# Performance work log

Measured on AMD Instinct MI355X. Metric: run time of the kernel, lower is better.

## Reference

```python
import jax, jax.numpy as jnp
import numpy as np

B, L, D = 4, 2048, 256
H, HD = 8, 64
MAX_LEN = 2048


def setup_inputs() -> dict:
    key = jax.random.key(0)
    ks = jax.random.split(key, 5)
    x = jax.random.normal(ks[0], (B, L, D), dtype=jnp.float32)
    glorot_q = (2.0 / (D + H * HD)) ** 0.5
    Wq = jax.random.normal(ks[1], (D, H * HD), dtype=jnp.float32) * glorot_q
    Wk = jax.random.normal(ks[2], (D, H * HD), dtype=jnp.float32) * glorot_q
    bq = jnp.zeros((H, 1, 1, HD), dtype=jnp.float32)
    bk = jnp.zeros((H, 1, 1, HD), dtype=jnp.float32)
    prior_mean = jax.random.uniform(ks[3], (H,), dtype=jnp.float32, minval=-1.0, maxval=1.0)
    log_prior_std = jnp.full((H,), np.log(0.4), dtype=jnp.float32)
    return {"x": x, "Wq": Wq, "bq": bq, "Wk": Wk, "bk": bk,
            "prior_mean": prior_mean, "log_prior_std": log_prior_std,
            "max_length": MAX_LEN}


def _gaussian(x, mean, std):
    return 1.0 / std / jnp.sqrt(2.0 * 3.1415926) * jnp.exp(-0.5 * (x - mean) ** 2 / std ** 2)


def reference(x, Wq, bq, Wk, bk, prior_mean, log_prior_std, max_length):
    b, l, d = x.shape
    h, hd = bq.shape[0], bq.shape[-1]
    # normalized signed distance matrix [l, l]
    r = jnp.arange(l, dtype=jnp.float32)
    dist = (r[None, :] - r[:, None]) / float(max_length)
    # projections -> [h, b, l, hd] (split heads along last dim, heads leading)
    q = (x @ Wq).reshape(b, l, h, hd).transpose(2, 0, 1, 3) + bq
    k = (x @ Wk).reshape(b, l, h, hd).transpose(2, 0, 1, 3) + bk
    # gaussian positional prior per head [h, l, l]
    prior = _gaussian(dist[None, :, :], prior_mean[:, None, None],
                      jnp.exp(log_prior_std)[:, None, None])
    # scaled QK^T * prior -> softmax over keys
    scores = jnp.einsum('hbqd,hbkd->hbqk', q, k) * (float(hd) ** -0.5)
    att = jax.nn.softmax(scores * prior[:, None, :, :], axis=-1)
    # distance-weighted reduction instead of V-matmul: [h, b, l] -> [b, l, h]
    distance = jnp.einsum('hbqk,qk->hbq', att, dist)
    return distance.transpose(1, 2, 0)
```

## Files before the change

kernel.cpp:

```cpp
#include <hip/hip_runtime.h>
#include <math.h>


#define B_  4
#define L_  2048
#define D_  256
#define H_  8
#define HD_ 64

typedef unsigned int u32;
typedef unsigned short u16;
typedef short bf16x8 __attribute__((ext_vector_type(8)));
typedef float f32x4  __attribute__((ext_vector_type(4)));

union U16x8 { u16 u[8]; bf16x8 v; uint4 q; };

__device__ __forceinline__ u16 bf16rne(float v) {
    u32 u = __float_as_uint(v);
    return (u16)((u + 0x7fffu + ((u >> 16) & 1u)) >> 16);
}
__device__ __forceinline__ float bf2f(u16 h) { return __uint_as_float(((u32)h) << 16); }

__global__ __launch_bounds__(256, 4) void proj_kernel(
    const float* __restrict__ x,
    const float* __restrict__ Wq, const float* __restrict__ bq,
    const float* __restrict__ Wk, const float* __restrict__ bk,
    u16* __restrict__ Qhi, u16* __restrict__ Qlo,
    u16* __restrict__ Khi, u16* __restrict__ Klo)
{
    __shared__ __align__(16) u16 Bs[2][64][40];

    const int z = blockIdx.z;
    const float* W    = z ? Wk : Wq;
    const float* bias = z ? bk : bq;
    u16* Ohi = z ? Khi : Qhi;
    u16* Olo = z ? Klo : Qlo;

    const int t = threadIdx.x, w = t >> 6, l = t & 63;
    const int kc = l & 15, lhi = l >> 4;
    const int m0 = blockIdx.x * 128 + w * 32;
    const int h  = blockIdx.y;

    const float* xp0 = x + (size_t)(m0 + kc) * D_;
    const float* xp1 = x + (size_t)(m0 + 16 + kc) * D_;

    f32x4 acc[2][4];
    #pragma unroll
    for (int mf = 0; mf < 2; ++mf)
        #pragma unroll
        for (int nf = 0; nf < 4; ++nf) acc[mf][nf] = (f32x4){0.f, 0.f, 0.f, 0.f};

    for (int ks = 0; ks < 8; ++ks) {
        __syncthreads();
        #pragma unroll
        for (int j = 0; j < 2; ++j) {
            const int fid = t + j * 256;
            const int kr = fid >> 4, c4 = fid & 15;
            float4 v = *(const float4*)&W[(size_t)(ks*32 + kr) * 512 + h*64 + c4*4];
            float vv[4] = {v.x, v.y, v.z, v.w};
            #pragma unroll
            for (int e = 0; e < 4; ++e) {
                const int n = c4*4 + e;
                const u16 hi = bf16rne(vv[e]);
                Bs[0][n][kr] = hi;
                Bs[1][n][kr] = bf16rne(vv[e] - bf2f(hi));
            }
        }
        __syncthreads();

        U16x8 ah[2], al[2];
        #pragma unroll
        for (int mf = 0; mf < 2; ++mf) {
            const float* xp = mf ? xp1 : xp0;
            float4 a = *(const float4*)(xp + ks*32 + lhi*8);
            float4 b = *(const float4*)(xp + ks*32 + lhi*8 + 4);
            float vv[8] = {a.x, a.y, a.z, a.w, b.x, b.y, b.z, b.w};
            #pragma unroll
            for (int e = 0; e < 8; ++e) {
                const u16 hi = bf16rne(vv[e]);
                ah[mf].u[e] = hi;
                al[mf].u[e] = bf16rne(vv[e] - bf2f(hi));
            }
        }

        #pragma unroll
        for (int nf = 0; nf < 4; ++nf) {
            const bf16x8 bh = *(const bf16x8*)&Bs[0][nf*16 + kc][lhi*8];
            const bf16x8 bl = *(const bf16x8*)&Bs[1][nf*16 + kc][lhi*8];
            #pragma unroll
            for (int mf = 0; mf < 2; ++mf) {
                acc[mf][nf] = __builtin_amdgcn_mfma_f32_16x16x32_bf16(ah[mf].v, bh, acc[mf][nf], 0, 0, 0);
                acc[mf][nf] = __builtin_amdgcn_mfma_f32_16x16x32_bf16(ah[mf].v, bl, acc[mf][nf], 0, 0, 0);
                acc[mf][nf] = __builtin_amdgcn_mfma_f32_16x16x32_bf16(al[mf].v, bh, acc[mf][nf], 0, 0, 0);
            }
        }
    }

    #pragma unroll
    for (int mf = 0; mf < 2; ++mf)
        #pragma unroll
        for (int nf = 0; nf < 4; ++nf) {
            const float bv = bias[h * 64 + nf*16 + kc];
            #pragma unroll
            for (int r = 0; r < 4; ++r) {
                const float v = acc[mf][nf][r] + bv;
                const u16 hi = bf16rne(v);
                const u16 lo = bf16rne(v - bf2f(hi));
                const int m = m0 + mf*16 + lhi*4 + r;
                const int bb = m >> 11, ll = m & (L_ - 1);
                const size_t o = (((size_t)h * B_ + bb) * L_ + ll) * HD_ + nf*16 + kc;
                Ohi[o] = hi; Olo[o] = lo;
            }
        }
}

__global__ __launch_bounds__(512, 4) void attn_kernel(
    const u16* __restrict__ Qhi, const u16* __restrict__ Qlo,
    const u16* __restrict__ Khi, const u16* __restrict__ Klo,
    const float* __restrict__ prior_mean, const float* __restrict__ log_prior_std,
    const int* __restrict__ max_len, float* __restrict__ out)
{
    __shared__ __align__(16) u16 kls[2][64 * 64];
    __shared__ float2 Ptab[2176];

    const int t = threadIdx.x, w = t >> 6, l = t & 63;
    const int kc = l & 15, lhi = l >> 4;
    const int q0 = blockIdx.x * 128;
    const int hb = blockIdx.y, h = hb >> 2, b = hb & 3;
    const int qw = q0 + w * 16;

    const float iml = 1.0f / (float)(*max_len);
    const float mu  = prior_mean[h];
    const float sg  = __expf(log_prior_std[h]);
    const float isg = 1.0f / sg;
    const float coef = 0.125f / (sg * 2.5066282746310002f) * 1.44269504089f;
    for (int i = t; i < 2175; i += 512) {
        const float dist = (float)(i - q0 - 127) * iml;
        const float tt = (dist - mu) * isg;
        Ptab[i] = make_float2(coef * __expf(-0.5f * tt * tt), dist);
    }

    bf16x8 qh[2], ql2[2];
    #pragma unroll
    for (int dh = 0; dh < 2; ++dh) {
        const size_t qo = ((size_t)hb * L_ + qw + kc) * HD_ + dh*32 + lhi*8;
        qh[dh]  = *(const bf16x8*)&Qhi[qo];
        ql2[dh] = *(const bf16x8*)&Qlo[qo];
    }

    const float2* pbase = &Ptab[lhi*4 + 127 - w*16 - kc];

    const int spl = t >> 8;
    const int srow = (t & 255) >> 2;
    const int sq = t & 3;
    const int sr7 = srow & 7;
    const u16* Kg = (spl ? Klo : Khi) + ((size_t)hb * L_ + srow) * HD_ + sq * 16;
    u16* lds_row = &kls[spl][srow * 64];

    const int sl0 = lhi ^ (l & 7);
    const int sl1 = (4 + lhi) ^ (l & 7);

    float lv = 0.f, wv = 0.f;

    for (int kt = 0; kt < 32; ++kt) {
        __syncthreads();
        {
            const u16* src = Kg + (size_t)kt * 64 * HD_;
            const uint4 g0 = *(const uint4*)src;
            const uint4 g1 = *(const uint4*)(src + 8);
            const int p0 = (sq*2)     ^ sr7;
            const int p1 = (sq*2 + 1) ^ sr7;
            *(uint4*)&lds_row[p0 * 8] = g0;
            *(uint4*)&lds_row[p1 * 8] = g1;
        }
        __syncthreads();

        f32x4 acc[4];
        #pragma unroll
        for (int kf = 0; kf < 4; ++kf) acc[kf] = (f32x4){0.f, 0.f, 0.f, 0.f};

        #pragma unroll
        for (int kf = 0; kf < 4; ++kf) {
            const int rbase = (kf*16 + kc) * 64;
            const bf16x8 ah0 = *(const bf16x8*)&kls[0][rbase + sl0*8];
            const bf16x8 ah1 = *(const bf16x8*)&kls[0][rbase + sl1*8];
            const bf16x8 al0 = *(const bf16x8*)&kls[1][rbase + sl0*8];
            const bf16x8 al1 = *(const bf16x8*)&kls[1][rbase + sl1*8];
            acc[kf] = __builtin_amdgcn_mfma_f32_16x16x32_bf16(ah0, qh[0],  acc[kf], 0, 0, 0);
            acc[kf] = __builtin_amdgcn_mfma_f32_16x16x32_bf16(ah1, qh[1],  acc[kf], 0, 0, 0);
            acc[kf] = __builtin_amdgcn_mfma_f32_16x16x32_bf16(ah0, ql2[0], acc[kf], 0, 0, 0);
            acc[kf] = __builtin_amdgcn_mfma_f32_16x16x32_bf16(ah1, ql2[1], acc[kf], 0, 0, 0);
            acc[kf] = __builtin_amdgcn_mfma_f32_16x16x32_bf16(al0, qh[0],  acc[kf], 0, 0, 0);
            acc[kf] = __builtin_amdgcn_mfma_f32_16x16x32_bf16(al1, qh[1],  acc[kf], 0, 0, 0);
        }

        const float2* pp = pbase + kt * 64;
        #pragma unroll
        for (int kf = 0; kf < 4; ++kf)
            #pragma unroll
            for (int r = 0; r < 4; ++r) {
                const float2 pd = pp[kf*16 + r];
                const float e = exp2f(acc[kf][r] * pd.x);
                lv += e;
                wv = fmaf(e, pd.y, wv);
            }
    }

    lv += __shfl_xor(lv, 16); wv += __shfl_xor(wv, 16);
    lv += __shfl_xor(lv, 32); wv += __shfl_xor(wv, 32);
    if (lhi == 0) {
        const int q = qw + kc;
        out[((size_t)(b * L_ + q)) * H_ + h] = wv / lv;
    }
}

extern "C" void kernel_launch(void* const* d_in, const int* in_sizes, int n_in,
                              void* d_out, int out_size, void* d_ws, size_t ws_size,
                              hipStream_t stream)
{
    const float* x   = (const float*)d_in[0];
    const float* Wq  = (const float*)d_in[1];
    const float* bq  = (const float*)d_in[2];
    const float* Wk  = (const float*)d_in[3];
    const float* bk  = (const float*)d_in[4];
    const float* pm  = (const float*)d_in[5];
    const float* lps = (const float*)d_in[6];
    const int*   mlp = (const int*)d_in[7];
    float* out = (float*)d_out;

    u16* Qhi = (u16*)d_ws;
    u16* Qlo = Qhi + 4194304;
    u16* Khi = Qlo + 4194304;
    u16* Klo = Khi + 4194304;

    proj_kernel<<<dim3(64, 8, 2), 256, 0, stream>>>(x, Wq, bq, Wk, bk, Qhi, Qlo, Khi, Klo);
    attn_kernel<<<dim3(16, 32), 512, 0, stream>>>(Qhi, Qlo, Khi, Klo, pm, lps, mlp, out);
}
```

Before: 163.4 us.

## Pre-split x/W to bf16 pairs, double-buffer K tiles, remap blocks per XCD

A new prep kernel converts x and a transposed W into bf16 hi/lo pairs once, so the projection kernel reads them straight from global memory with no LDS staging or per-block conversion. This path is taken only when the workspace is large enough, otherwise the old projection kernel runs. The attention kernel double-buffers K tiles in LDS with register prefetch and one barrier per tile. It also drops the distance table by computing the weighted sum algebraically, uses a raw exp2 builtin with setprio around the MFMA block, and remaps block indices so each XCD handles contiguous head/batch work. Together these cut LDS traffic and conversion work, at the cost of an extra launch, more workspace and more LDS.

```diff
diff --git a/kernel.cpp b/kernel.cpp
--- a/kernel.cpp
+++ b/kernel.cpp
@@ -13,36 +13,92 @@
 typedef short bf16x8 __attribute__((ext_vector_type(8)));
 typedef float f32x4  __attribute__((ext_vector_type(4)));
 
-union U16x8 { u16 u[8]; bf16x8 v; uint4 q; };
-
 __device__ __forceinline__ u16 bf16rne(float v) {
     u32 u = __float_as_uint(v);
     return (u16)((u + 0x7fffu + ((u >> 16) & 1u)) >> 16);
 }
 __device__ __forceinline__ float bf2f(u16 h) { return __uint_as_float(((u32)h) << 16); }
 
-__global__ __launch_bounds__(256, 4) void proj_kernel(
-    const float* __restrict__ x,
-    const float* __restrict__ Wq, const float* __restrict__ bq,
-    const float* __restrict__ Wk, const float* __restrict__ bk,
+#if __has_builtin(__builtin_amdgcn_exp2f)
+__device__ __forceinline__ float fast_exp2(float x) { return __builtin_amdgcn_exp2f(x); }
+#else
+__device__ __forceinline__ float fast_exp2(float x) { return exp2f(x); }
+#endif
+
+__global__ __launch_bounds__(256) void prep_kernel(
+    const float* __restrict__ x, const float* __restrict__ Wq, const float* __restrict__ Wk,
+    u16* __restrict__ xhi, u16* __restrict__ xlo,
+    u16* __restrict__ wthi, u16* __restrict__ wtlo)
+{
+    __shared__ float Ws[64][65];
+    const int t = threadIdx.x;
+    if (blockIdx.x < 1024) {
+        const size_t base = ((size_t)blockIdx.x * 256 + t) * 8;
+        float4 a = *(const float4*)&x[base];
+        float4 b = *(const float4*)&x[base + 4];
+        float v[8] = {a.x, a.y, a.z, a.w, b.x, b.y, b.z, b.w};
+        u32 hp[4], lp[4];
+        #pragma unroll
+        for (int j = 0; j < 4; ++j) {
+            u16 h0 = bf16rne(v[2*j]),   l0 = bf16rne(v[2*j]   - bf2f(bf16rne(v[2*j])));
+            u16 h1 = bf16rne(v[2*j+1]), l1 = bf16rne(v[2*j+1] - bf2f(bf16rne(v[2*j+1])));
+            hp[j] = (u32)h0 | ((u32)h1 << 16);
+            lp[j] = (u32)l0 | ((u32)l1 << 16);
+        }
+        *(uint4*)&xhi[base] = *(uint4*)hp;
+        *(uint4*)&xlo[base] = *(uint4*)lp;
+    } else {
+        const int widx = blockIdx.x - 1024;
+        const int wsel = widx >> 5;
+        const float* W = wsel ? Wk : Wq;
+        const int tile = widx & 31;
+        const int kt = tile >> 3, nt = tile & 7;
+        const int kr = t >> 2, c4 = t & 3;
+        #pragma unroll
+        for (int c = 0; c < 4; ++c) {
+            float4 v = *(const float4*)&W[(size_t)(kt*64 + kr) * 512 + nt*64 + c4*16 + c*4];
+            Ws[kr][c4*16 + c*4 + 0] = v.x; Ws[kr][c4*16 + c*4 + 1] = v.y;
+            Ws[kr][c4*16 + c*4 + 2] = v.z; Ws[kr][c4*16 + c*4 + 3] = v.w;
+        }
+        __syncthreads();
+        const int nr = t >> 2;
+        const int kc4 = (t & 3) * 16;
+        u32 hp[8], lp[8];
+        #pragma unroll
+        for (int j = 0; j < 8; ++j) {
+            float v0 = Ws[kc4 + 2*j][nr], v1 = Ws[kc4 + 2*j + 1][nr];
+            u16 h0 = bf16rne(v0), h1 = bf16rne(v1);
+            u16 l0 = bf16rne(v0 - bf2f(h0)), l1 = bf16rne(v1 - bf2f(h1));
+            hp[j] = (u32)h0 | ((u32)h1 << 16);
+            lp[j] = (u32)l0 | ((u32)l1 << 16);
+        }
+        const size_t ob = ((size_t)wsel*512 + nt*64 + nr) * 256 + kt*64 + kc4;
+        *(uint4*)&wthi[ob] = *(uint4*)&hp[0]; *(uint4*)&wthi[ob + 8] = *(uint4*)&hp[4];
+        *(uint4*)&wtlo[ob] = *(uint4*)&lp[0]; *(uint4*)&wtlo[ob + 8] = *(uint4*)&lp[4];
+    }
+}
+
+__global__ __launch_bounds__(256, 4) void projA_kernel(
+    const u16* __restrict__ xhi, const u16* __restrict__ xlo,
+    const u16* __restrict__ wthi, const u16* __restrict__ wtlo,
+    const float* __restrict__ bq, const float* __restrict__ bk,
     u16* __restrict__ Qhi, u16* __restrict__ Qlo,
     u16* __restrict__ Khi, u16* __restrict__ Klo)
 {
-    __shared__ __align__(16) u16 Bs[2][64][40];
-
-    const int z = blockIdx.z;
-    const float* W    = z ? Wk : Wq;
+    const int p = blockIdx.x;
+    const int xcd = p & 7, s = p >> 3;
+    const int mx = xcd * 8 + (s & 7);
+    const int hz = s >> 3;
+    const int h = hz & 7, z = hz >> 3;
+
     const float* bias = z ? bk : bq;
     u16* Ohi = z ? Khi : Qhi;
     u16* Olo = z ? Klo : Qlo;
 
     const int t = threadIdx.x, w = t >> 6, l = t & 63;
     const int kc = l & 15, lhi = l >> 4;
-    const int m0 = blockIdx.x * 128 + w * 32;
-    const int h  = blockIdx.y;
-
-    const float* xp0 = x + (size_t)(m0 + kc) * D_;
-    const float* xp1 = x + (size_t)(m0 + 16 + kc) * D_;
+    const int m0 = mx * 128 + w * 32;
+    const size_t wb = ((size_t)z * 512 + h * 64) * 256;
 
     f32x4 acc[2][4];
     #pragma unroll
@@ -50,50 +106,30 @@
         #pragma unroll
         for (int nf = 0; nf < 4; ++nf) acc[mf][nf] = (f32x4){0.f, 0.f, 0.f, 0.f};
 
+    #pragma unroll 2
     for (int ks = 0; ks < 8; ++ks) {
-        __syncthreads();
-        #pragma unroll
-        for (int j = 0; j < 2; ++j) {
-            const int fid = t + j * 256;
-            const int kr = fid >> 4, c4 = fid & 15;
-            float4 v = *(const float4*)&W[(size_t)(ks*32 + kr) * 512 + h*64 + c4*4];
-            float vv[4] = {v.x, v.y, v.z, v.w};
-            #pragma unroll
-            for (int e = 0; e < 4; ++e) {
-                const int n = c4*4 + e;
-                const u16 hi = bf16rne(vv[e]);
-                Bs[0][n][kr] = hi;
-                Bs[1][n][kr] = bf16rne(vv[e] - bf2f(hi));
-            }
-        }
-        __syncthreads();
-
-        U16x8 ah[2], al[2];
+        const int ko = ks * 32 + lhi * 8;
+        bf16x8 ah[2], al[2], bh[4], bl[4];
         #pragma unroll
         for (int mf = 0; mf < 2; ++mf) {
-            const float* xp = mf ? xp1 : xp0;
-            float4 a = *(const float4*)(xp + ks*32 + lhi*8);
-            float4 b = *(const float4*)(xp + ks*32 + lhi*8 + 4);
-            float vv[8] = {a.x, a.y, a.z, a.w, b.x, b.y, b.z, b.w};
-            #pragma unroll
-            for (int e = 0; e < 8; ++e) {
-                const u16 hi = bf16rne(vv[e]);
-                ah[mf].u[e] = hi;
-                al[mf].u[e] = bf16rne(vv[e] - bf2f(hi));
-            }
-        }
-
+            const size_t ao = (size_t)(m0 + mf*16 + kc) * 256 + ko;
+            ah[mf] = *(const bf16x8*)&xhi[ao];
+            al[mf] = *(const bf16x8*)&xlo[ao];
+        }
         #pragma unroll
         for (int nf = 0; nf < 4; ++nf) {
-            const bf16x8 bh = *(const bf16x8*)&Bs[0][nf*16 + kc][lhi*8];
-            const bf16x8 bl = *(const bf16x8*)&Bs[1][nf*16 + kc][lhi*8];
-            #pragma unroll
-            for (int mf = 0; mf < 2; ++mf) {
-                acc[mf][nf] = __builtin_amdgcn_mfma_f32_16x16x32_bf16(ah[mf].v, bh, acc[mf][nf], 0, 0, 0);
-                acc[mf][nf] = __builtin_amdgcn_mfma_f32_16x16x32_bf16(ah[mf].v, bl, acc[mf][nf], 0, 0, 0);
-                acc[mf][nf] = __builtin_amdgcn_mfma_f32_16x16x32_bf16(al[mf].v, bh, acc[mf][nf], 0, 0, 0);
-            }
-        }
+            const size_t bo = wb + (size_t)(nf*16 + kc) * 256 + ko;
+            bh[nf] = *(const bf16x8*)&wthi[bo];
+            bl[nf] = *(const bf16x8*)&wtlo[bo];
+        }
+        #pragma unroll
+        for (int mf = 0; mf < 2; ++mf)
+            #pragma unroll
+            for (int nf = 0; nf < 4; ++nf) {
+                acc[mf][nf] = __builtin_amdgcn_mfma_f32_16x16x32_bf16(ah[mf], bh[nf], acc[mf][nf], 0, 0, 0);
+                acc[mf][nf] = __builtin_amdgcn_mfma_f32_16x16x32_bf16(ah[mf], bl[nf], acc[mf][nf], 0, 0, 0);
+                acc[mf][nf] = __builtin_amdgcn_mfma_f32_16x16x32_bf16(al[mf], bh[nf], acc[mf][nf], 0, 0, 0);
+            }
     }
 
     #pragma unroll
@@ -114,30 +150,127 @@
         }
 }
 
+__global__ __launch_bounds__(256, 4) void projB_kernel(
+    const float* __restrict__ x,
+    const float* __restrict__ Wq, const float* __restrict__ bq,
+    const float* __restrict__ Wk, const float* __restrict__ bk,
+    u16* __restrict__ Qhi, u16* __restrict__ Qlo,
+    u16* __restrict__ Khi, u16* __restrict__ Klo)
+{
+    __shared__ __align__(16) u16 Bs[2][64][40];
+
+    const int z = blockIdx.z;
+    const float* W    = z ? Wk : Wq;
+    const float* bias = z ? bk : bq;
+    u16* Ohi = z ? Khi : Qhi;
+    u16* Olo = z ? Klo : Qlo;
+
+    const int t = threadIdx.x, w = t >> 6, l = t & 63;
+    const int kc = l & 15, lhi = l >> 4;
+    const int m0 = blockIdx.x * 128 + w * 32;
+    const int h  = blockIdx.y;
+
+    const float* xp0 = x + (size_t)(m0 + kc) * D_;
+    const float* xp1 = x + (size_t)(m0 + 16 + kc) * D_;
+
+    f32x4 acc[2][4];
+    #pragma unroll
+    for (int mf = 0; mf < 2; ++mf)
+        #pragma unroll
+        for (int nf = 0; nf < 4; ++nf) acc[mf][nf] = (f32x4){0.f, 0.f, 0.f, 0.f};
+
+    for (int ks = 0; ks < 8; ++ks) {
+        __syncthreads();
+        #pragma unroll
+        for (int j = 0; j < 2; ++j) {
+            const int fid = t + j * 256;
+            const int kr = fid >> 4, c4 = fid & 15;
+            float4 v = *(const float4*)&W[(size_t)(ks*32 + kr) * 512 + h*64 + c4*4];
+            float vv[4] = {v.x, v.y, v.z, v.w};
+            #pragma unroll
+            for (int e = 0; e < 4; ++e) {
+                const int n = c4*4 + e;
+                const u16 hi = bf16rne(vv[e]);
+                Bs[0][n][kr] = hi;
+                Bs[1][n][kr] = bf16rne(vv[e] - bf2f(hi));
+            }
+        }
+        __syncthreads();
+
+        union { u16 u[8]; bf16x8 v; } ah[2], al[2];
+        #pragma unroll
+        for (int mf = 0; mf < 2; ++mf) {
+            const float* xp = mf ? xp1 : xp0;
+            float4 a = *(const float4*)(xp + ks*32 + lhi*8);
+            float4 b = *(const float4*)(xp + ks*32 + lhi*8 + 4);
+            float vv[8] = {a.x, a.y, a.z, a.w, b.x, b.y, b.z, b.w};
+            #pragma unroll
+            for (int e = 0; e < 8; ++e) {
+                const u16 hi = bf16rne(vv[e]);
+                ah[mf].u[e] = hi;
+                al[mf].u[e] = bf16rne(vv[e] - bf2f(hi));
+            }
+        }
+
+        #pragma unroll
+        for (int nf = 0; nf < 4; ++nf) {
+            const bf16x8 bh = *(const bf16x8*)&Bs[0][nf*16 + kc][lhi*8];
+            const bf16x8 bl = *(const bf16x8*)&Bs[1][nf*16 + kc][lhi*8];
+            #pragma unroll
+            for (int mf = 0; mf < 2; ++mf) {
+                acc[mf][nf] = __builtin_amdgcn_mfma_f32_16x16x32_bf16(ah[mf].v, bh, acc[mf][nf], 0, 0, 0);
+                acc[mf][nf] = __builtin_amdgcn_mfma_f32_16x16x32_bf16(ah[mf].v, bl, acc[mf][nf], 0, 0, 0);
+                acc[mf][nf] = __builtin_amdgcn_mfma_f32_16x16x32_bf16(al[mf].v, bh, acc[mf][nf], 0, 0, 0);
+            }
+        }
+    }
+
+    #pragma unroll
+    for (int mf = 0; mf < 2; ++mf)
+        #pragma unroll
+        for (int nf = 0; nf < 4; ++nf) {
+            const float bv = bias[h * 64 + nf*16 + kc];
+            #pragma unroll
+            for (int r = 0; r < 4; ++r) {
+                const float v = acc[mf][nf][r] + bv;
+                const u16 hi = bf16rne(v);
+                const u16 lo = bf16rne(v - bf2f(hi));
+                const int m = m0 + mf*16 + lhi*4 + r;
+                const int bb = m >> 11, ll = m & (L_ - 1);
+                const size_t o = (((size_t)h * B_ + bb) * L_ + ll) * HD_ + nf*16 + kc;
+                Ohi[o] = hi; Olo[o] = lo;
+            }
+        }
+}
+
 __global__ __launch_bounds__(512, 4) void attn_kernel(
     const u16* __restrict__ Qhi, const u16* __restrict__ Qlo,
     const u16* __restrict__ Khi, const u16* __restrict__ Klo,
     const float* __restrict__ prior_mean, const float* __restrict__ log_prior_std,
     const int* __restrict__ max_len, float* __restrict__ out)
 {
-    __shared__ __align__(16) u16 kls[2][64 * 64];
-    __shared__ float2 Ptab[2176];
+    __shared__ __align__(16) u16 kls[2][2][64 * 64];
+    __shared__ float Ptab[2176];
 
     const int t = threadIdx.x, w = t >> 6, l = t & 63;
     const int kc = l & 15, lhi = l >> 4;
-    const int q0 = blockIdx.x * 128;
-    const int hb = blockIdx.y, h = hb >> 2, b = hb & 3;
+
+    const int p = blockIdx.x;
+    const int xcd = p & 7, s = p >> 3;
+    const int hb = xcd * 4 + (s >> 4);
+    const int q0 = (s & 15) * 128;
+    const int h = hb >> 2, b = hb & 3;
     const int qw = q0 + w * 16;
 
     const float iml = 1.0f / (float)(*max_len);
     const float mu  = prior_mean[h];
     const float sg  = __expf(log_prior_std[h]);
     const float isg = 1.0f / sg;
-    const float coef = 0.125f / (sg * 2.5066282746310002f) * 1.44269504089f;
+    const float coef = 0.125f * 1.44269504089f / (sg * 2.5066282746310002f);
     for (int i = t; i < 2175; i += 512) {
         const float dist = (float)(i - q0 - 127) * iml;
         const float tt = (dist - mu) * isg;
-        Ptab[i] = make_float2(coef * __expf(-0.5f * tt * tt), dist);
+        Ptab[i] = coef * __expf(-0.5f * tt * tt);
     }
 
     bf16x8 qh[2], ql2[2];
@@ -148,69 +281,83 @@
         ql2[dh] = *(const bf16x8*)&Qlo[qo];
     }
 
-    const float2* pbase = &Ptab[lhi*4 + 127 - w*16 - kc];
+    const float* pb = &Ptab[lhi*4 + 127 - w*16 - kc];
+    const float dqf = (float)(lhi*4 - qw - kc);
 
     const int spl = t >> 8;
     const int srow = (t & 255) >> 2;
     const int sq = t & 3;
     const int sr7 = srow & 7;
     const u16* Kg = (spl ? Klo : Khi) + ((size_t)hb * L_ + srow) * HD_ + sq * 16;
-    u16* lds_row = &kls[spl][srow * 64];
-
-    const int sl0 = lhi ^ (l & 7);
-    const int sl1 = (4 + lhi) ^ (l & 7);
-
-    float lv = 0.f, wv = 0.f;
-
-    for (int kt = 0; kt < 32; ++kt) {
-        __syncthreads();
-        {
-            const u16* src = Kg + (size_t)kt * 64 * HD_;
-            const uint4 g0 = *(const uint4*)src;
-            const uint4 g1 = *(const uint4*)(src + 8);
-            const int p0 = (sq*2)     ^ sr7;
-            const int p1 = (sq*2 + 1) ^ sr7;
-            *(uint4*)&lds_row[p0 * 8] = g0;
-            *(uint4*)&lds_row[p1 * 8] = g1;
-        }
-        __syncthreads();
-
-        f32x4 acc[4];
-        #pragma unroll
-        for (int kf = 0; kf < 4; ++kf) acc[kf] = (f32x4){0.f, 0.f, 0.f, 0.f};
-
-        #pragma unroll
-        for (int kf = 0; kf < 4; ++kf) {
-            const int rbase = (kf*16 + kc) * 64;
-            const bf16x8 ah0 = *(const bf16x8*)&kls[0][rbase + sl0*8];
-            const bf16x8 ah1 = *(const bf16x8*)&kls[0][rbase + sl1*8];
-            const bf16x8 al0 = *(const bf16x8*)&kls[1][rbase + sl0*8];
-            const bf16x8 al1 = *(const bf16x8*)&kls[1][rbase + sl1*8];
-            acc[kf] = __builtin_amdgcn_mfma_f32_16x16x32_bf16(ah0, qh[0],  acc[kf], 0, 0, 0);
-            acc[kf] = __builtin_amdgcn_mfma_f32_16x16x32_bf16(ah1, qh[1],  acc[kf], 0, 0, 0);
-            acc[kf] = __builtin_amdgcn_mfma_f32_16x16x32_bf16(ah0, ql2[0], acc[kf], 0, 0, 0);
-            acc[kf] = __builtin_amdgcn_mfma_f32_16x16x32_bf16(ah1, ql2[1], acc[kf], 0, 0, 0);
-            acc[kf] = __builtin_amdgcn_mfma_f32_16x16x32_bf16(al0, qh[0],  acc[kf], 0, 0, 0);
-            acc[kf] = __builtin_amdgcn_mfma_f32_16x16x32_bf16(al1, qh[1],  acc[kf], 0, 0, 0);
-        }
-
-        const float2* pp = pbase + kt * 64;
-        #pragma unroll
-        for (int kf = 0; kf < 4; ++kf)
-            #pragma unroll
-            for (int r = 0; r < 4; ++r) {
-                const float2 pd = pp[kf*16 + r];
-                const float e = exp2f(acc[kf][r] * pd.x);
-                lv += e;
-                wv = fmaf(e, pd.y, wv);
-            }
-    }
-
-    lv += __shfl_xor(lv, 16); wv += __shfl_xor(wv, 16);
-    lv += __shfl_xor(lv, 32); wv += __shfl_xor(wv, 32);
+    const int p0 = ((sq*2)     ^ sr7) * 8;
+    const int p1 = ((sq*2 + 1) ^ sr7) * 8;
+    u16* wdst0 = &kls[0][spl][srow * 64];
+    u16* wdst1 = &kls[1][spl][srow * 64];
+
+    const int sl0 = (lhi ^ (kc & 7)) * 8;
+    const int sl1 = ((4 + lhi) ^ (kc & 7)) * 8;
+
+    float lv = 0.f, wvs = 0.f;
+
+    uint4 ra0, ra1, rb0, rb1;
+    ra0 = *(const uint4*)Kg; ra1 = *(const uint4*)(Kg + 8);
+    *(uint4*)&wdst0[p0] = ra0; *(uint4*)&wdst0[p1] = ra1;
+    ra0 = *(const uint4*)(Kg + 4096); ra1 = *(const uint4*)(Kg + 4096 + 8);
+    __syncthreads();
+
+#define LOADT(RX0, RX1, TI) { const u16* src_ = Kg + (size_t)(TI) * 4096; \
+    RX0 = *(const uint4*)src_; RX1 = *(const uint4*)(src_ + 8); }
+#define WRT(DST, RX0, RX1) { *(uint4*)&DST[p0] = RX0; *(uint4*)&DST[p1] = RX1; }
+#define CTILE(TI, BS) { \
+    const u16* bh_ = &kls[BS][0][0]; const u16* bl_ = &kls[BS][1][0]; \
+    f32x4 acc[4]; \
+    _Pragma("unroll") for (int kf = 0; kf < 4; ++kf) acc[kf] = (f32x4){0.f,0.f,0.f,0.f}; \
+    __builtin_amdgcn_s_setprio(1); \
+    _Pragma("unroll") for (int kf = 0; kf < 4; ++kf) { \
+        const int rb_ = (kf*16 + kc) * 64; \
+        const bf16x8 ah0 = *(const bf16x8*)&bh_[rb_ + sl0]; \
+        const bf16x8 ah1 = *(const bf16x8*)&bh_[rb_ + sl1]; \
+        const bf16x8 al0 = *(const bf16x8*)&bl_[rb_ + sl0]; \
+        const bf16x8 al1 = *(const bf16x8*)&bl_[rb_ + sl1]; \
+        acc[kf] = __builtin_amdgcn_mfma_f32_16x16x32_bf16(ah0, qh[0],  acc[kf], 0, 0, 0); \
+        acc[kf] = __builtin_amdgcn_mfma_f32_16x16x32_bf16(ah1, qh[1],  acc[kf], 0, 0, 0); \
+        acc[kf] = __builtin_amdgcn_mfma_f32_16x16x32_bf16(ah0, ql2[0], acc[kf], 0, 0, 0); \
+        acc[kf] = __builtin_amdgcn_mfma_f32_16x16x32_bf16(ah1, ql2[1], acc[kf], 0, 0, 0); \
+        acc[kf] = __builtin_amdgcn_mfma_f32_16x16x32_bf16(al0, qh[0],  acc[kf], 0, 0, 0); \
+        acc[kf] = __builtin_amdgcn_mfma_f32_16x16x32_bf16(al1, qh[1],  acc[kf], 0, 0, 0); \
+    } \
+    __builtin_amdgcn_s_setprio(0); \
+    const float* pp = pb + (TI) * 64; \
+    float S0 = 0.f, S1 = 0.f; \
+    _Pragma("unroll") for (int kf = 0; kf < 4; ++kf) \
+        _Pragma("unroll") for (int r = 0; r < 4; ++r) { \
+            const int cc = kf*16 + r; \
+            const float e = fast_exp2(acc[kf][r] * pp[cc]); \
+            S0 += e; if (cc) S1 = fmaf(e, (float)cc, S1); \
+        } \
+    lv += S0; \
+    wvs = fmaf((float)((TI) << 6) + dqf, S0, wvs + S1); \
+}
+
+    for (int kt = 0; kt < 32; kt += 2) {
+        if (kt + 2 < 32) LOADT(rb0, rb1, kt + 2);
+        WRT(wdst1, ra0, ra1);
+        CTILE(kt, 0);
+        __syncthreads();
+        if (kt + 3 < 32) LOADT(ra0, ra1, kt + 3);
+        if (kt + 2 < 32) WRT(wdst0, rb0, rb1);
+        CTILE(kt + 1, 1);
+        __syncthreads();
+    }
+#undef LOADT
+#undef WRT
+#undef CTILE
+
+    lv  += __shfl_xor(lv, 16);  wvs += __shfl_xor(wvs, 16);
+    lv  += __shfl_xor(lv, 32);  wvs += __shfl_xor(wvs, 32);
     if (lhi == 0) {
         const int q = qw + kc;
-        out[((size_t)(b * L_ + q)) * H_ + h] = wv / lv;
+        out[((size_t)(b * L_ + q)) * H_ + h] = (wvs * iml) / lv;
     }
 }
 
@@ -233,6 +380,17 @@
     u16* Khi = Qlo + 4194304;
     u16* Klo = Khi + 4194304;
 
-    proj_kernel<<<dim3(64, 8, 2), 256, 0, stream>>>(x, Wq, bq, Wk, bk, Qhi, Qlo, Khi, Klo);
-    attn_kernel<<<dim3(16, 32), 512, 0, stream>>>(Qhi, Qlo, Khi, Klo, pm, lps, mlp, out);
-}
+    if (ws_size >= (size_t)41 * 1024 * 1024) {
+        u16* xhi  = Klo + 4194304;
+        u16* xlo  = xhi + 2097152;
+        u16* wthi = xlo + 2097152;
+        u16* wtlo = wthi + 262144;
+        prep_kernel<<<dim3(1088), 256, 0, stream>>>(x, Wq, Wk, xhi, xlo, wthi, wtlo);
+        projA_kernel<<<dim3(1024), 256, 0, stream>>>(xhi, xlo, wthi, wtlo, bq, bk,
+                                                     Qhi, Qlo, Khi, Klo);
+    } else {
+        projB_kernel<<<dim3(64, 8, 2), 256, 0, stream>>>(x, Wq, bq, Wk, bk,
+                                                         Qhi, Qlo, Khi, Klo);
+    }
+    attn_kernel<<<dim3(512), 512, 0, stream>>>(Qhi, Qlo, Khi, Klo, pm, lps, mlp, out);
+}
```

After: 178.6 us. +9.3%, slower.
